# Performance work log

Measured on AMD Instinct MI355X. Metric: run time of the kernel, lower is better.

## Reference

```python
import jax, jax.numpy as jnp
import numpy as np

B = 65536      # total rows = env_batch(8192) * n_slave(8)
DIN = 256      # input_shape
H = 64         # slave_hidden_dim
A = 32         # attention_dim
NACT = 14      # n_actions
NS = 8         # n_slave


def setup_inputs() -> dict:
    key = jax.random.key(0)
    ks = jax.random.split(key, 12)
    s = 0.05
    return {
        "obs": jax.random.normal(ks[0], (B, DIN), jnp.float32),
        "hidden_state": jax.random.normal(ks[1], (B, H), jnp.float32),
        "enc_W": jax.random.normal(ks[2], (DIN, H), jnp.float32) * s,
        "enc_b": jnp.zeros((H,), jnp.float32),
        "gru_Wih": jax.random.normal(ks[3], (3 * H, H), jnp.float32) * s,
        "gru_Whh": jax.random.normal(ks[4], (3 * H, H), jnp.float32) * s,
        "gru_bih": jnp.zeros((3 * H,), jnp.float32),
        "gru_bhh": jnp.zeros((3 * H,), jnp.float32),
        "qW": jax.random.normal(ks[5], (H, A), jnp.float32) * s,
        "kW": jax.random.normal(ks[6], (H, A), jnp.float32) * s,
        "vW": jax.random.normal(ks[7], (H, A), jnp.float32) * s,
        "vb": jnp.zeros((A,), jnp.float32),
        "decW": jax.random.normal(ks[8], (H + A, NACT), jnp.float32) * s,
        "decb": jnp.zeros((NACT,), jnp.float32),
        "n_slave": NS,
    }


def reference(obs, hidden_state, enc_W, enc_b, gru_Wih, gru_Whh, gru_bih, gru_bhh,
              qW, kW, vW, vb, decW, decb, n_slave):
    # encoding + ReLU
    x = jax.nn.relu(obs @ enc_W + enc_b)                      # [B, H]
    # torch GRUCell: r,z,n gate order in weight rows
    gx = x @ gru_Wih.T + gru_bih                              # [B, 3H]
    gh = hidden_state @ gru_Whh.T + gru_bhh                   # [B, 3H]
    xr, xz, xn = jnp.split(gx, 3, axis=-1)
    hr, hz, hn = jnp.split(gh, 3, axis=-1)
    r = jax.nn.sigmoid(xr + hr)
    z = jax.nn.sigmoid(xz + hz)
    n = jnp.tanh(xn + r * hn)
    h_out = (1.0 - z) * n + z * hidden_state                  # [B, H]

    Ad = qW.shape[-1]
    q = (h_out @ qW).reshape(-1, n_slave, Ad)                 # [b, n, A]
    k = (h_out @ kW).reshape(-1, n_slave, Ad)
    v = jax.nn.relu(h_out @ vW + vb).reshape(-1, n_slave, Ad)

    # exclude-self attention == diagonal-masked softmax attention
    scores = jnp.einsum('bia,bja->bij', q, k) / jnp.sqrt(jnp.float32(Ad))
    eye = jnp.eye(n_slave, dtype=bool)
    scores = jnp.where(eye, jnp.float32(-1e9), scores)
    attn = jax.nn.softmax(scores, axis=-1)                    # [b, n, n]
    xatt = jnp.einsum('bij,bja->bia', attn, v).reshape(-1, Ad)  # [B, A]

    out = jnp.concatenate([h_out, xatt], axis=-1) @ decW + decb  # [B, n_actions]
    return (out, h_out)
```

## Files before the change

kernel.cpp:

```cpp
#include <hip/hip_runtime.h>
#include <hip/hip_bf16.h>


#define DIN   256
#define H     64
#define A_DIM 32
#define NACT  14
#define MBLK  64
#define BTOT  65536

typedef unsigned int u32;
typedef unsigned short u16;
using short8 = __attribute__((ext_vector_type(8))) short;
using f32x4  = __attribute__((ext_vector_type(4))) float;

__device__ __forceinline__ u32 f2bf(float f){
  u32 x = __float_as_uint(f);
  return (x + 0x7fffu + ((x >> 16) & 1u)) >> 16;
}
__device__ __forceinline__ float bf2f(u16 u){ return __uint_as_float(((u32)u) << 16); }
__device__ __forceinline__ u32 pk2(float a, float b){ return f2bf(a) | (f2bf(b) << 16); }
__device__ __forceinline__ float sigm(float x){ return 1.0f / (1.0f + __expf(-x)); }
__device__ __forceinline__ float tanhp(float x){ return 1.0f - 2.0f / (__expf(2.0f * x) + 1.0f); }

#define MFMA16(a,b,c) __builtin_amdgcn_mfma_f32_16x16x32_bf16((a),(b),(c),0,0,0)


__global__ __launch_bounds__(256, 3)
void commslave_mfma(const float* __restrict__ obs,
                    const float* __restrict__ hid,
                    const float* __restrict__ encW,
                    const float* __restrict__ encb,
                    const float* __restrict__ Wih,
                    const float* __restrict__ Whh,
                    const float* __restrict__ bih,
                    const float* __restrict__ bhh,
                    const float* __restrict__ qW,
                    const float* __restrict__ kW,
                    const float* __restrict__ vW,
                    const float* __restrict__ vb,
                    const float* __restrict__ decW,
                    const float* __restrict__ decb,
                    float* __restrict__ out)
{
  __shared__ __align__(16) u16 ldsU[26624];
  float* R0f = (float*)ldsU;

  const int tid  = threadIdx.x;
  const int lane = tid & 63;
  const int w    = tid >> 6;
  const int quad = lane >> 4;
  const int l16  = lane & 15;
  const int M0   = 16 * w;
  const size_t rowbase = (size_t)blockIdx.x * MBLK;

  const float4* obs4 = (const float4*)(obs + rowbase * DIN);
  const float4* hid4 = (const float4*)hid;

  f32x4 ce[4];
  #pragma unroll
  for (int t = 0; t < 4; t++) ce[t] = (f32x4){0.f,0.f,0.f,0.f};

  #pragma unroll 1
  for (int half = 0; half < 2; half++) {
    if (half == 1) __syncthreads();
    #pragma unroll
    for (int i = 0; i < 8; i++) {
      int idx = tid + 256 * i;
      int row = idx >> 5, c4 = idx & 31;
      float4 v = obs4[row * 64 + half * 32 + c4];
      *(uint2*)&ldsU[row * 136 + c4 * 4] = make_uint2(pk2(v.x, v.y), pk2(v.z, v.w));
    }
    #pragma unroll
    for (int i = 0; i < 8; i++) {
      int idx = tid + 256 * i;
      int row = idx >> 4, c4 = idx & 15;
      float4 v = ((const float4*)encW)[(half * 128 + row) * 16 + c4];
      u16* p = &ldsU[8704 + (4 * c4) * 136 + row];
      p[0]       = f2bf(v.x);
      p[136]     = f2bf(v.y);
      p[272]     = f2bf(v.z);
      p[408]     = f2bf(v.w);
    }
    if (half == 0) {
      #pragma unroll
      for (int i = 0; i < 4; i++) {
        int idx = tid + 256 * i;
        int row = idx >> 4, c4 = idx & 15;
        float4 v = hid4[(rowbase + row) * 16 + c4];
        *(uint2*)&ldsU[22016 + row * 72 + c4 * 4] = make_uint2(pk2(v.x, v.y), pk2(v.z, v.w));
      }
    }
    __syncthreads();
    #pragma unroll
    for (int ks = 0; ks < 4; ks++) {
      short8 a = *(const short8*)&ldsU[(M0 + l16) * 136 + ks * 32 + quad * 8];
      #pragma unroll
      for (int t = 0; t < 4; t++) {
        short8 b = *(const short8*)&ldsU[8704 + (16 * t + l16) * 136 + ks * 32 + quad * 8];
        ce[t] = MFMA16(a, b, ce[t]);
      }
    }
  }
  #pragma unroll
  for (int t = 0; t < 4; t++) {
    float bias = encb[16 * t + l16];
    #pragma unroll
    for (int r = 0; r < 4; r++) {
      float xv = fmaxf(ce[t][r] + bias, 0.f);
      ldsU[17408 + (M0 + quad * 4 + r) * 72 + 16 * t + l16] = f2bf(xv);
    }
  }
  __syncthreads();

  #pragma unroll
  for (int i = 0; i < 12; i++) {
    int idx = tid + 256 * i;
    int row = idx >> 4, c4 = idx & 15;
    float4 v = ((const float4*)Wih)[row * 16 + c4];
    *(uint2*)&ldsU[row * 72 + c4 * 4] = make_uint2(pk2(v.x, v.y), pk2(v.z, v.w));
  }
  __syncthreads();
  f32x4 gxr[12];
  #pragma unroll
  for (int t = 0; t < 12; t++) gxr[t] = (f32x4){0.f,0.f,0.f,0.f};
  #pragma unroll
  for (int ks = 0; ks < 2; ks++) {
    short8 a = *(const short8*)&ldsU[17408 + (M0 + l16) * 72 + ks * 32 + quad * 8];
    #pragma unroll
    for (int t = 0; t < 12; t++) {
      short8 b = *(const short8*)&ldsU[(16 * t + l16) * 72 + ks * 32 + quad * 8];
      gxr[t] = MFMA16(a, b, gxr[t]);
    }
  }
  __syncthreads();
  #pragma unroll
  for (int i = 0; i < 12; i++) {
    int idx = tid + 256 * i;
    int row = idx >> 4, c4 = idx & 15;
    float4 v = ((const float4*)Whh)[row * 16 + c4];
    *(uint2*)&ldsU[row * 72 + c4 * 4] = make_uint2(pk2(v.x, v.y), pk2(v.z, v.w));
  }
  __syncthreads();
  f32x4 ghr[12];
  #pragma unroll
  for (int t = 0; t < 12; t++) ghr[t] = (f32x4){0.f,0.f,0.f,0.f};
  #pragma unroll
  for (int ks = 0; ks < 2; ks++) {
    short8 a = *(const short8*)&ldsU[22016 + (M0 + l16) * 72 + ks * 32 + quad * 8];
    #pragma unroll
    for (int t = 0; t < 12; t++) {
      short8 b = *(const short8*)&ldsU[(16 * t + l16) * 72 + ks * 32 + quad * 8];
      ghr[t] = MFMA16(a, b, ghr[t]);
    }
  }
  __syncthreads();

  {
    const float* Ws[3] = {qW, kW, vW};
    #pragma unroll
    for (int mtx = 0; mtx < 3; mtx++) {
      const float4* W4 = (const float4*)Ws[mtx];
      #pragma unroll
      for (int i = 0; i < 2; i++) {
        int idx = tid + 256 * i;
        int k = idx >> 3, c4 = idx & 7;
        float4 v = W4[k * 8 + c4];
        u16* p = &ldsU[(mtx * 32 + 4 * c4) * 72 + k];
        p[0]   = f2bf(v.x);
        p[72]  = f2bf(v.y);
        p[144] = f2bf(v.z);
        p[216] = f2bf(v.w);
      }
    }
  }
  {
    float* outH = out + (size_t)BTOT * NACT;
    #pragma unroll
    for (int u = 0; u < 4; u++) {
      int n = 16 * u + l16;
      float bri = bih[n],       brh = bhh[n];
      float bzi = bih[64 + n],  bzh = bhh[64 + n];
      float bni = bih[128 + n], bnh = bhh[128 + n];
      #pragma unroll
      for (int r = 0; r < 4; r++) {
        int m = M0 + quad * 4 + r;
        float rg = sigm((gxr[u][r]     + bri) + (ghr[u][r]     + brh));
        float zg = sigm((gxr[4+u][r]   + bzi) + (ghr[4+u][r]   + bzh));
        float nn = tanhp((gxr[8+u][r]  + bni) + rg * (ghr[8+u][r] + bnh));
        float hp = bf2f(ldsU[22016 + m * 72 + n]);
        float ho = (1.f - zg) * nn + zg * hp;
        outH[(rowbase + m) * H + n] = ho;
        ldsU[22016 + m * 72 + n] = f2bf(ho);
      }
    }
  }
  __syncthreads();

  f32x4 cq[6];
  #pragma unroll
  for (int t = 0; t < 6; t++) cq[t] = (f32x4){0.f,0.f,0.f,0.f};
  #pragma unroll
  for (int ks = 0; ks < 2; ks++) {
    short8 a = *(const short8*)&ldsU[22016 + (M0 + l16) * 72 + ks * 32 + quad * 8];
    #pragma unroll
    for (int t = 0; t < 6; t++) {
      short8 b = *(const short8*)&ldsU[(16 * t + l16) * 72 + ks * 32 + quad * 8];
      cq[t] = MFMA16(a, b, cq[t]);
    }
  }
  __syncthreads();

  {
    const float qs = 0.17677669529663687f;
    #pragma unroll
    for (int t = 0; t < 6; t++) {
      int col = 16 * t + l16;
      float add = (t >= 4) ? vb[col - 64] : 0.f;
      #pragma unroll
      for (int r = 0; r < 4; r++) {
        float vv = cq[t][r] + add;
        if (t < 2) vv *= qs;
        if (t >= 4) vv = fmaxf(vv, 0.f);
        R0f[(M0 + quad * 4 + r) * 104 + col] = vv;
      }
    }
    #pragma unroll
    for (int i = 0; i < 6; i++) {
      int idx = tid + 256 * i;
      int k = idx >> 4, n = idx & 15;
      float val = (n < 14) ? decW[k * NACT + n] : 0.f;
      ldsU[13312 + n * 104 + k] = f2bf(val);
    }
  }
  __syncthreads();

  {
    const int r  = tid >> 2;
    const int s4 = tid & 3;
    const int gb = r & ~7, ri = r & 7;
    const float* fq = &R0f[r * 104];
    float sc[2];
    #pragma unroll
    for (int jj = 0; jj < 2; jj++) {
      int j = s4 + 4 * jj;
      const float* fk = &R0f[(gb + j) * 104 + 32];
      float d = 0.f;
      #pragma unroll
      for (int a4 = 0; a4 < 32; a4 += 4) {
        float4 q4 = *(const float4*)&fq[a4];
        float4 k4 = *(const float4*)&fk[a4];
        d += q4.x*k4.x + q4.y*k4.y + q4.z*k4.z + q4.w*k4.w;
      }
      sc[jj] = (j == ri) ? -1e30f : d;
    }
    float m = fmaxf(sc[0], sc[1]);
    m = fmaxf(m, __shfl_xor(m, 1, 4));
    m = fmaxf(m, __shfl_xor(m, 2, 4));
    float p0 = (s4     == ri) ? 0.f : __expf(sc[0] - m);
    float p1 = (s4 + 4 == ri) ? 0.f : __expf(sc[1] - m);
    float sum = p0 + p1;
    sum += __shfl_xor(sum, 1, 4);
    sum += __shfl_xor(sum, 2, 4);
    float inv = 1.f / sum;
    R0f[r * 104 + 96 + s4]     = p0 * inv;
    R0f[r * 104 + 96 + s4 + 4] = p1 * inv;
    float xa[8] = {0,0,0,0,0,0,0,0};
    #pragma unroll
    for (int j = 0; j < 8; j++) {
      float aj = R0f[r * 104 + 96 + j];
      const float* fv = &R0f[(gb + j) * 104 + 64 + s4 * 8];
      #pragma unroll
      for (int u = 0; u < 8; u++) xa[u] += aj * fv[u];
    }
    *(uint4*)&ldsU[17408 + r * 72 + s4 * 8] =
        make_uint4(pk2(xa[0], xa[1]), pk2(xa[2], xa[3]),
                   pk2(xa[4], xa[5]), pk2(xa[6], xa[7]));
  }
  __syncthreads();

  {
    f32x4 co = (f32x4){0.f,0.f,0.f,0.f};
    #pragma unroll
    for (int ks = 0; ks < 3; ks++) {
      short8 a;
      if (ks < 2) a = *(const short8*)&ldsU[22016 + (M0 + l16) * 72 + ks * 32 + quad * 8];
      else        a = *(const short8*)&ldsU[17408 + (M0 + l16) * 72 + quad * 8];
      short8 b = *(const short8*)&ldsU[13312 + l16 * 104 + ks * 32 + quad * 8];
      co = MFMA16(a, b, co);
    }
    if (l16 < NACT) {
      float bias = decb[l16];
      #pragma unroll
      for (int r = 0; r < 4; r++) {
        int m = M0 + quad * 4 + r;
        out[(rowbase + m) * NACT + l16] = co[r] + bias;
      }
    }
  }
}

extern "C" void kernel_launch(void* const* d_in, const int* in_sizes, int n_in,
                              void* d_out, int out_size, void* d_ws, size_t ws_size,
                              hipStream_t stream) {
  (void)in_sizes; (void)n_in; (void)d_ws; (void)ws_size; (void)out_size;
  const float* obs  = (const float*)d_in[0];
  const float* hid  = (const float*)d_in[1];
  const float* encW = (const float*)d_in[2];
  const float* encb = (const float*)d_in[3];
  const float* Wih  = (const float*)d_in[4];
  const float* Whh  = (const float*)d_in[5];
  const float* bih  = (const float*)d_in[6];
  const float* bhh  = (const float*)d_in[7];
  const float* qW   = (const float*)d_in[8];
  const float* kW   = (const float*)d_in[9];
  const float* vW   = (const float*)d_in[10];
  const float* vb   = (const float*)d_in[11];
  const float* decW = (const float*)d_in[12];
  const float* decb = (const float*)d_in[13];
  float* out = (float*)d_out;

  commslave_mfma<<<BTOT / MBLK, 256, 0, stream>>>(
      obs, hid, encW, encb, Wih, Whh, bih, bhh, qW, kW, vW, vb, decW, decb, out);
}
```

Measured before the change: 155.9 us.

## Pre-convert weights once in a prep kernel and stream operands from global memory

A small prep kernel now converts all weights to bf16 in MFMA-friendly transposed layouts in a global buffer and folds the GRU biases together. The main kernel reads B operands straight from that buffer instead of staging them in LDS per block. It loads obs and hidden A operands directly into registers, fuses the gx/gh GRU matmuls per column tile, and scopes the attention per wave. This removes per-block weight conversion, most LDS staging and many block barriers, at the cost of an extra launch and global/L2 reads of weights from every wave.

```diff
diff --git a/kernel.cpp b/kernel.cpp
--- a/kernel.cpp
+++ b/kernel.cpp
@@ -1,50 +1,70 @@
 #include <hip/hip_runtime.h>
-#include <hip/hip_bf16.h>
-
-
-#define DIN   256
-#define H     64
-#define A_DIM 32
-#define NACT  14
-#define MBLK  64
-#define BTOT  65536
-
-typedef unsigned int u32;
+
+
+#define NACT 14
+#define BTOT 65536
+
+typedef unsigned int  u32;
 typedef unsigned short u16;
 using short8 = __attribute__((ext_vector_type(8))) short;
 using f32x4  = __attribute__((ext_vector_type(4))) float;
 
+#define ENCB 0
+#define WIHB 16896
+#define WHHB 30720
+#define QKVB 44544
+#define DECB 51456
+#define WTOT 53120
+
+__device__ u16   g_wbuf[WTOT];
+__device__ float g_bias[256];
+
 __device__ __forceinline__ u32 f2bf(float f){
   u32 x = __float_as_uint(f);
   return (x + 0x7fffu + ((x >> 16) & 1u)) >> 16;
 }
-__device__ __forceinline__ float bf2f(u16 u){ return __uint_as_float(((u32)u) << 16); }
 __device__ __forceinline__ u32 pk2(float a, float b){ return f2bf(a) | (f2bf(b) << 16); }
 __device__ __forceinline__ float sigm(float x){ return 1.0f / (1.0f + __expf(-x)); }
 __device__ __forceinline__ float tanhp(float x){ return 1.0f - 2.0f / (__expf(2.0f * x) + 1.0f); }
+__device__ __forceinline__ short8 as_s8(uint4 v){ union { uint4 u; short8 s; } x; x.u = v; return x.s; }
 
 #define MFMA16(a,b,c) __builtin_amdgcn_mfma_f32_16x16x32_bf16((a),(b),(c),0,0,0)
 
+__global__ void prep(const float* __restrict__ encW, const float* __restrict__ Wih,
+                     const float* __restrict__ Whh,  const float* __restrict__ qW,
+                     const float* __restrict__ kW,   const float* __restrict__ vW,
+                     const float* __restrict__ decW, const float* __restrict__ bih,
+                     const float* __restrict__ bhh)
+{
+  int i = blockIdx.x * 256 + threadIdx.x;
+  if (blockIdx.x == 0) {
+    int n = threadIdx.x & 63, g = threadIdx.x >> 6;
+    float v;
+    if      (g == 0) v = bih[n]       + bhh[n];
+    else if (g == 1) v = bih[64 + n]  + bhh[64 + n];
+    else if (g == 2) v = bih[128 + n];
+    else             v = bhh[128 + n];
+    g_bias[threadIdx.x] = v;
+  }
+  if (i >= WTOT) return;
+  float val = 0.f;
+  if (i < WIHB)      { int n = i / 264, k = i % 264;            if (k < 256) val = encW[k * 64 + n]; }
+  else if (i < WHHB) { int j = i - WIHB; int n = j / 72, k = j % 72; if (k < 64) val = Wih[n * 64 + k]; }
+  else if (i < QKVB) { int j = i - WHHB; int n = j / 72, k = j % 72; if (k < 64) val = Whh[n * 64 + k]; }
+  else if (i < DECB) { int j = i - QKVB; int n = j / 72, k = j % 72;
+    if (k < 64) { int m = n >> 5, nn = n & 31;
+      val = (m == 0) ? qW[k * 32 + nn] * 0.17677669529663687f
+          : (m == 1) ? kW[k * 32 + nn] : vW[k * 32 + nn]; } }
+  else { int j = i - DECB; int n = j / 104, k = j % 104; if (n < 14 && k < 96) val = decW[k * 14 + n]; }
+  g_wbuf[i] = (u16)f2bf(val);
+}
 
 __global__ __launch_bounds__(256, 3)
-void commslave_mfma(const float* __restrict__ obs,
-                    const float* __restrict__ hid,
-                    const float* __restrict__ encW,
-                    const float* __restrict__ encb,
-                    const float* __restrict__ Wih,
-                    const float* __restrict__ Whh,
-                    const float* __restrict__ bih,
-                    const float* __restrict__ bhh,
-                    const float* __restrict__ qW,
-                    const float* __restrict__ kW,
-                    const float* __restrict__ vW,
-                    const float* __restrict__ vb,
-                    const float* __restrict__ decW,
-                    const float* __restrict__ decb,
-                    float* __restrict__ out)
+void commslave_main(const float* __restrict__ obs,  const float* __restrict__ hid,
+                    const float* __restrict__ encb, const float* __restrict__ vb,
+                    const float* __restrict__ decb, float* __restrict__ out)
 {
-  __shared__ __align__(16) u16 ldsU[26624];
-  float* R0f = (float*)ldsU;
+  __shared__ __align__(16) u16 ldsU[23040];
 
   const int tid  = threadIdx.x;
   const int lane = tid & 63;
@@ -52,250 +72,173 @@
   const int quad = lane >> 4;
   const int l16  = lane & 15;
   const int M0   = 16 * w;
-  const size_t rowbase = (size_t)blockIdx.x * MBLK;
-
-  const float4* obs4 = (const float4*)(obs + rowbase * DIN);
-  const float4* hid4 = (const float4*)hid;
+  const int gr   = blockIdx.x * 64 + M0;
+
+  float* Sf = (float*)(ldsU + 9216) + w * (16 * 68);
+  float* Af = (float*)(ldsU + 9216) + w * (16 * 108);
 
   f32x4 ce[4];
   #pragma unroll
-  for (int t = 0; t < 4; t++) ce[t] = (f32x4){0.f,0.f,0.f,0.f};
-
-  #pragma unroll 1
-  for (int half = 0; half < 2; half++) {
-    if (half == 1) __syncthreads();
-    #pragma unroll
-    for (int i = 0; i < 8; i++) {
-      int idx = tid + 256 * i;
-      int row = idx >> 5, c4 = idx & 31;
-      float4 v = obs4[row * 64 + half * 32 + c4];
-      *(uint2*)&ldsU[row * 136 + c4 * 4] = make_uint2(pk2(v.x, v.y), pk2(v.z, v.w));
-    }
-    #pragma unroll
-    for (int i = 0; i < 8; i++) {
-      int idx = tid + 256 * i;
-      int row = idx >> 4, c4 = idx & 15;
-      float4 v = ((const float4*)encW)[(half * 128 + row) * 16 + c4];
-      u16* p = &ldsU[8704 + (4 * c4) * 136 + row];
-      p[0]       = f2bf(v.x);
-      p[136]     = f2bf(v.y);
-      p[272]     = f2bf(v.z);
-      p[408]     = f2bf(v.w);
-    }
-    if (half == 0) {
+  for (int t = 0; t < 4; t++) { float bv = encb[16 * t + l16]; ce[t] = (f32x4){bv, bv, bv, bv}; }
+  #pragma unroll
+  for (int ks = 0; ks < 8; ks++) {
+    const float* ap = obs + (size_t)(gr + l16) * 256 + ks * 32 + quad * 8;
+    float4 a0 = *(const float4*)ap, a1 = *(const float4*)(ap + 4);
+    short8 a = as_s8(make_uint4(pk2(a0.x, a0.y), pk2(a0.z, a0.w), pk2(a1.x, a1.y), pk2(a1.z, a1.w)));
+    #pragma unroll
+    for (int t = 0; t < 4; t++) {
+      short8 b = as_s8(*(const uint4*)&g_wbuf[ENCB + (16 * t + l16) * 264 + ks * 32 + quad * 8]);
+      ce[t] = MFMA16(a, b, ce[t]);
+    }
+  }
+  #pragma unroll
+  for (int t = 0; t < 4; t++)
+    #pragma unroll
+    for (int r = 0; r < 4; r++)
+      Sf[(quad * 4 + r) * 68 + 16 * t + l16] = fmaxf(ce[t][r], 0.f);
+  #pragma unroll
+  for (int i = 0; i < 2; i++) {
+    int c = lane + 64 * i, lr = c >> 3, j = c & 7;
+    const float* sp = &Sf[lr * 68 + 8 * j];
+    float4 v0 = *(const float4*)sp, v1 = *(const float4*)(sp + 4);
+    *(uint4*)&ldsU[(M0 + lr) * 72 + 8 * j] =
+        make_uint4(pk2(v0.x, v0.y), pk2(v0.z, v0.w), pk2(v1.x, v1.y), pk2(v1.z, v1.w));
+  }
+  __syncthreads();
+
+  short8 ax[2], ah[2];
+  #pragma unroll
+  for (int ks = 0; ks < 2; ks++) {
+    ax[ks] = *(const short8*)&ldsU[(M0 + l16) * 72 + ks * 32 + quad * 8];
+    const float* hp = hid + (size_t)(gr + l16) * 64 + ks * 32 + quad * 8;
+    float4 h0 = *(const float4*)hp, h1 = *(const float4*)(hp + 4);
+    ah[ks] = as_s8(make_uint4(pk2(h0.x, h0.y), pk2(h0.z, h0.w), pk2(h1.x, h1.y), pk2(h1.z, h1.w)));
+  }
+  #pragma unroll
+  for (int u = 0; u < 4; u++) {
+    f32x4 g6[6];
+    #pragma unroll
+    for (int t = 0; t < 6; t++) g6[t] = (f32x4){0.f, 0.f, 0.f, 0.f};
+    #pragma unroll
+    for (int g = 0; g < 3; g++) {
+      int row = 64 * g + 16 * u + l16;
       #pragma unroll
-      for (int i = 0; i < 4; i++) {
-        int idx = tid + 256 * i;
-        int row = idx >> 4, c4 = idx & 15;
-        float4 v = hid4[(rowbase + row) * 16 + c4];
-        *(uint2*)&ldsU[22016 + row * 72 + c4 * 4] = make_uint2(pk2(v.x, v.y), pk2(v.z, v.w));
+      for (int ks = 0; ks < 2; ks++) {
+        short8 bi = as_s8(*(const uint4*)&g_wbuf[WIHB + row * 72 + ks * 32 + quad * 8]);
+        g6[g] = MFMA16(ax[ks], bi, g6[g]);
+        short8 bh = as_s8(*(const uint4*)&g_wbuf[WHHB + row * 72 + ks * 32 + quad * 8]);
+        g6[3 + g] = MFMA16(ah[ks], bh, g6[3 + g]);
       }
     }
-    __syncthreads();
-    #pragma unroll
-    for (int ks = 0; ks < 4; ks++) {
-      short8 a = *(const short8*)&ldsU[(M0 + l16) * 136 + ks * 32 + quad * 8];
-      #pragma unroll
-      for (int t = 0; t < 4; t++) {
-        short8 b = *(const short8*)&ldsU[8704 + (16 * t + l16) * 136 + ks * 32 + quad * 8];
-        ce[t] = MFMA16(a, b, ce[t]);
-      }
-    }
-  }
-  #pragma unroll
-  for (int t = 0; t < 4; t++) {
-    float bias = encb[16 * t + l16];
+    int nc = 16 * u + l16;
+    float brz = g_bias[nc], bzz = g_bias[64 + nc], bni = g_bias[128 + nc], bnh = g_bias[192 + nc];
     #pragma unroll
     for (int r = 0; r < 4; r++) {
-      float xv = fmaxf(ce[t][r] + bias, 0.f);
-      ldsU[17408 + (M0 + quad * 4 + r) * 72 + 16 * t + l16] = f2bf(xv);
-    }
+      float hp = hid[(size_t)(gr + quad * 4 + r) * 64 + nc];
+      float rg = sigm(g6[0][r] + g6[3][r] + brz);
+      float zg = sigm(g6[1][r] + g6[4][r] + bzz);
+      float nn = tanhp(g6[2][r] + bni + rg * (g6[5][r] + bnh));
+      Sf[(quad * 4 + r) * 68 + nc] = (1.f - zg) * nn + zg * hp;
+    }
+  }
+  float* outH = out + (size_t)BTOT * NACT;
+  #pragma unroll
+  for (int i = 0; i < 2; i++) {
+    int c = lane + 64 * i, lr = c >> 3, j = c & 7;
+    const float* sp = &Sf[lr * 68 + 8 * j];
+    float4 v0 = *(const float4*)sp, v1 = *(const float4*)(sp + 4);
+    *(uint4*)&ldsU[4608 + (M0 + lr) * 72 + 8 * j] =
+        make_uint4(pk2(v0.x, v0.y), pk2(v0.z, v0.w), pk2(v1.x, v1.y), pk2(v1.z, v1.w));
+    *(float4*)(outH + (size_t)(gr + lr) * 64 + 8 * j)     = v0;
+    *(float4*)(outH + (size_t)(gr + lr) * 64 + 8 * j + 4) = v1;
   }
   __syncthreads();
 
-  #pragma unroll
-  for (int i = 0; i < 12; i++) {
-    int idx = tid + 256 * i;
-    int row = idx >> 4, c4 = idx & 15;
-    float4 v = ((const float4*)Wih)[row * 16 + c4];
-    *(uint2*)&ldsU[row * 72 + c4 * 4] = make_uint2(pk2(v.x, v.y), pk2(v.z, v.w));
-  }
-  __syncthreads();
-  f32x4 gxr[12];
-  #pragma unroll
-  for (int t = 0; t < 12; t++) gxr[t] = (f32x4){0.f,0.f,0.f,0.f};
-  #pragma unroll
-  for (int ks = 0; ks < 2; ks++) {
-    short8 a = *(const short8*)&ldsU[17408 + (M0 + l16) * 72 + ks * 32 + quad * 8];
-    #pragma unroll
-    for (int t = 0; t < 12; t++) {
-      short8 b = *(const short8*)&ldsU[(16 * t + l16) * 72 + ks * 32 + quad * 8];
-      gxr[t] = MFMA16(a, b, gxr[t]);
-    }
-  }
-  __syncthreads();
-  #pragma unroll
-  for (int i = 0; i < 12; i++) {
-    int idx = tid + 256 * i;
-    int row = idx >> 4, c4 = idx & 15;
-    float4 v = ((const float4*)Whh)[row * 16 + c4];
-    *(uint2*)&ldsU[row * 72 + c4 * 4] = make_uint2(pk2(v.x, v.y), pk2(v.z, v.w));
-  }
-  __syncthreads();
-  f32x4 ghr[12];
-  #pragma unroll
-  for (int t = 0; t < 12; t++) ghr[t] = (f32x4){0.f,0.f,0.f,0.f};
-  #pragma unroll
-  for (int ks = 0; ks < 2; ks++) {
-    short8 a = *(const short8*)&ldsU[22016 + (M0 + l16) * 72 + ks * 32 + quad * 8];
-    #pragma unroll
-    for (int t = 0; t < 12; t++) {
-      short8 b = *(const short8*)&ldsU[(16 * t + l16) * 72 + ks * 32 + quad * 8];
-      ghr[t] = MFMA16(a, b, ghr[t]);
-    }
-  }
-  __syncthreads();
+  short8 hx[2];
+  #pragma unroll
+  for (int ks = 0; ks < 2; ks++)
+    hx[ks] = *(const short8*)&ldsU[4608 + (M0 + l16) * 72 + ks * 32 + quad * 8];
+  f32x4 cq[6];
+  #pragma unroll
+  for (int t = 0; t < 6; t++) {
+    float bv = (t >= 4) ? vb[16 * (t - 4) + l16] : 0.f;
+    cq[t] = (f32x4){bv, bv, bv, bv};
+  }
+  #pragma unroll
+  for (int ks = 0; ks < 2; ks++)
+    #pragma unroll
+    for (int t = 0; t < 6; t++) {
+      short8 b = as_s8(*(const uint4*)&g_wbuf[QKVB + (16 * t + l16) * 72 + ks * 32 + quad * 8]);
+      cq[t] = MFMA16(hx[ks], b, cq[t]);
+    }
+  #pragma unroll
+  for (int t = 0; t < 6; t++)
+    #pragma unroll
+    for (int r = 0; r < 4; r++) {
+      float v = cq[t][r];
+      if (t >= 4) v = fmaxf(v, 0.f);
+      Af[(quad * 4 + r) * 108 + 16 * t + l16] = v;
+    }
 
   {
-    const float* Ws[3] = {qW, kW, vW};
-    #pragma unroll
-    for (int mtx = 0; mtx < 3; mtx++) {
-      const float4* W4 = (const float4*)Ws[mtx];
-      #pragma unroll
-      for (int i = 0; i < 2; i++) {
-        int idx = tid + 256 * i;
-        int k = idx >> 3, c4 = idx & 7;
-        float4 v = W4[k * 8 + c4];
-        u16* p = &ldsU[(mtx * 32 + 4 * c4) * 72 + k];
-        p[0]   = f2bf(v.x);
-        p[72]  = f2bf(v.y);
-        p[144] = f2bf(v.z);
-        p[216] = f2bf(v.w);
-      }
-    }
-  }
-  {
-    float* outH = out + (size_t)BTOT * NACT;
-    #pragma unroll
-    for (int u = 0; u < 4; u++) {
-      int n = 16 * u + l16;
-      float bri = bih[n],       brh = bhh[n];
-      float bzi = bih[64 + n],  bzh = bhh[64 + n];
-      float bni = bih[128 + n], bnh = bhh[128 + n];
-      #pragma unroll
-      for (int r = 0; r < 4; r++) {
-        int m = M0 + quad * 4 + r;
-        float rg = sigm((gxr[u][r]     + bri) + (ghr[u][r]     + brh));
-        float zg = sigm((gxr[4+u][r]   + bzi) + (ghr[4+u][r]   + bzh));
-        float nn = tanhp((gxr[8+u][r]  + bni) + rg * (ghr[8+u][r] + bnh));
-        float hp = bf2f(ldsU[22016 + m * 72 + n]);
-        float ho = (1.f - zg) * nn + zg * hp;
-        outH[(rowbase + m) * H + n] = ho;
-        ldsU[22016 + m * 72 + n] = f2bf(ho);
-      }
-    }
-  }
-  __syncthreads();
-
-  f32x4 cq[6];
-  #pragma unroll
-  for (int t = 0; t < 6; t++) cq[t] = (f32x4){0.f,0.f,0.f,0.f};
-  #pragma unroll
-  for (int ks = 0; ks < 2; ks++) {
-    short8 a = *(const short8*)&ldsU[22016 + (M0 + l16) * 72 + ks * 32 + quad * 8];
-    #pragma unroll
-    for (int t = 0; t < 6; t++) {
-      short8 b = *(const short8*)&ldsU[(16 * t + l16) * 72 + ks * 32 + quad * 8];
-      cq[t] = MFMA16(a, b, cq[t]);
-    }
-  }
-  __syncthreads();
-
-  {
-    const float qs = 0.17677669529663687f;
-    #pragma unroll
-    for (int t = 0; t < 6; t++) {
-      int col = 16 * t + l16;
-      float add = (t >= 4) ? vb[col - 64] : 0.f;
-      #pragma unroll
-      for (int r = 0; r < 4; r++) {
-        float vv = cq[t][r] + add;
-        if (t < 2) vv *= qs;
-        if (t >= 4) vv = fmaxf(vv, 0.f);
-        R0f[(M0 + quad * 4 + r) * 104 + col] = vv;
-      }
-    }
-    #pragma unroll
-    for (int i = 0; i < 6; i++) {
-      int idx = tid + 256 * i;
-      int k = idx >> 4, n = idx & 15;
-      float val = (n < 14) ? decW[k * NACT + n] : 0.f;
-      ldsU[13312 + n * 104 + k] = f2bf(val);
-    }
-  }
-  __syncthreads();
-
-  {
-    const int r  = tid >> 2;
-    const int s4 = tid & 3;
-    const int gb = r & ~7, ri = r & 7;
-    const float* fq = &R0f[r * 104];
+    const int r_l = lane >> 2, s4 = lane & 3;
+    const int gb = r_l & 8, ri = r_l & 7;
+    const float* fq = &Af[r_l * 108];
     float sc[2];
     #pragma unroll
     for (int jj = 0; jj < 2; jj++) {
       int j = s4 + 4 * jj;
-      const float* fk = &R0f[(gb + j) * 104 + 32];
+      const float* fk = &Af[(gb + j) * 108 + 32];
       float d = 0.f;
       #pragma unroll
       for (int a4 = 0; a4 < 32; a4 += 4) {
         float4 q4 = *(const float4*)&fq[a4];
         float4 k4 = *(const float4*)&fk[a4];
-        d += q4.x*k4.x + q4.y*k4.y + q4.z*k4.z + q4.w*k4.w;
+        d += q4.x * k4.x + q4.y * k4.y + q4.z * k4.z + q4.w * k4.w;
       }
       sc[jj] = (j == ri) ? -1e30f : d;
     }
     float m = fmaxf(sc[0], sc[1]);
-    m = fmaxf(m, __shfl_xor(m, 1, 4));
-    m = fmaxf(m, __shfl_xor(m, 2, 4));
+    m = fmaxf(m, __shfl_xor(m, 1));
+    m = fmaxf(m, __shfl_xor(m, 2));
     float p0 = (s4     == ri) ? 0.f : __expf(sc[0] - m);
     float p1 = (s4 + 4 == ri) ? 0.f : __expf(sc[1] - m);
     float sum = p0 + p1;
-    sum += __shfl_xor(sum, 1, 4);
-    sum += __shfl_xor(sum, 2, 4);
+    sum += __shfl_xor(sum, 1);
+    sum += __shfl_xor(sum, 2);
     float inv = 1.f / sum;
-    R0f[r * 104 + 96 + s4]     = p0 * inv;
-    R0f[r * 104 + 96 + s4 + 4] = p1 * inv;
-    float xa[8] = {0,0,0,0,0,0,0,0};
+    Af[r_l * 108 + 96 + s4]  = p0 * inv;
+    Af[r_l * 108 + 100 + s4] = p1 * inv;
+    float xa[8] = {0, 0, 0, 0, 0, 0, 0, 0};
     #pragma unroll
     for (int j = 0; j < 8; j++) {
-      float aj = R0f[r * 104 + 96 + j];
-      const float* fv = &R0f[(gb + j) * 104 + 64 + s4 * 8];
+      float aj = Af[r_l * 108 + 96 + j];
+      const float* fv = &Af[(gb + j) * 108 + 64 + 8 * s4];
+      float4 w0 = *(const float4*)fv, w1 = *(const float4*)(fv + 4);
+      xa[0] += aj * w0.x; xa[1] += aj * w0.y; xa[2] += aj * w0.z; xa[3] += aj * w0.w;
+      xa[4] += aj * w1.x; xa[5] += aj * w1.y; xa[6] += aj * w1.z; xa[7] += aj * w1.w;
+    }
+    *(uint4*)&ldsU[(M0 + r_l) * 72 + 8 * s4] =
+        make_uint4(pk2(xa[0], xa[1]), pk2(xa[2], xa[3]), pk2(xa[4], xa[5]), pk2(xa[6], xa[7]));
+  }
+  __syncthreads();
+
+  {
+    float db = (l16 < NACT) ? decb[l16] : 0.f;
+    f32x4 co = (f32x4){db, db, db, db};
+    #pragma unroll
+    for (int ks = 0; ks < 2; ks++) {
+      short8 a = *(const short8*)&ldsU[4608 + (M0 + l16) * 72 + ks * 32 + quad * 8];
+      short8 b = as_s8(*(const uint4*)&g_wbuf[DECB + l16 * 104 + ks * 32 + quad * 8]);
+      co = MFMA16(a, b, co);
+    }
+    short8 a2 = *(const short8*)&ldsU[(M0 + l16) * 72 + quad * 8];
+    short8 b2 = as_s8(*(const uint4*)&g_wbuf[DECB + l16 * 104 + 64 + quad * 8]);
+    co = MFMA16(a2, b2, co);
+    if (l16 < NACT) {
       #pragma unroll
-      for (int u = 0; u < 8; u++) xa[u] += aj * fv[u];
-    }
-    *(uint4*)&ldsU[17408 + r * 72 + s4 * 8] =
-        make_uint4(pk2(xa[0], xa[1]), pk2(xa[2], xa[3]),
-                   pk2(xa[4], xa[5]), pk2(xa[6], xa[7]));
-  }
-  __syncthreads();
-
-  {
-    f32x4 co = (f32x4){0.f,0.f,0.f,0.f};
-    #pragma unroll
-    for (int ks = 0; ks < 3; ks++) {
-      short8 a;
-      if (ks < 2) a = *(const short8*)&ldsU[22016 + (M0 + l16) * 72 + ks * 32 + quad * 8];
-      else        a = *(const short8*)&ldsU[17408 + (M0 + l16) * 72 + quad * 8];
-      short8 b = *(const short8*)&ldsU[13312 + l16 * 104 + ks * 32 + quad * 8];
-      co = MFMA16(a, b, co);
-    }
-    if (l16 < NACT) {
-      float bias = decb[l16];
-      #pragma unroll
-      for (int r = 0; r < 4; r++) {
-        int m = M0 + quad * 4 + r;
-        out[(rowbase + m) * NACT + l16] = co[r] + bias;
-      }
+      for (int r = 0; r < 4; r++)
+        out[(size_t)(gr + quad * 4 + r) * NACT + l16] = co[r];
     }
   }
 }
@@ -320,6 +263,6 @@
   const float* decb = (const float*)d_in[13];
   float* out = (float*)d_out;
 
-  commslave_mfma<<<BTOT / MBLK, 256, 0, stream>>>(
-      obs, hid, encW, encb, Wih, Whh, bih, bhh, qW, kW, vW, vb, decW, decb, out);
-}
+  prep<<<(WTOT + 255) / 256, 256, 0, stream>>>(encW, Wih, Whh, qW, kW, vW, decW, bih, bhh);
+  commslave_main<<<BTOT / 64, 256, 0, stream>>>(obs, hid, encb, vb, decb, out);
+}
```

New measurement: 163.3 us. 1.05x slower.
